# Performance work log

Hardware: AMD Instinct MI355X
Metric: run time of the kernel (lower is better)

## Reference

```python
import jax, jax.numpy as jnp
import numpy as np
from jax import lax

EPS_LN = 1e-5
EPS_NORM = 1e-12

def conv1x1(x, w):
    # x: [b,c,h,w], w: [o,c]
    return jnp.einsum('oc,bchw->bohw', w, x)

def dwconv3x3(x, w):
    # depthwise 3x3, w: [c,1,3,3]
    return lax.conv_general_dilated(
        x, w, window_strides=(1, 1), padding=[(1, 1), (1, 1)],
        feature_group_count=x.shape[1],
        dimension_numbers=('NCHW', 'OIHW', 'NCHW'))

def layernorm_chan(x, w, b):
    # WithBias LayerNorm over channel dim of NCHW (torch does it in b,(hw),c layout)
    mu = jnp.mean(x, axis=1, keepdims=True)
    var = jnp.mean((x - mu) ** 2, axis=1, keepdims=True)
    xn = (x - mu) / jnp.sqrt(var + EPS_LN)
    return xn * w[None, :, None, None] + b[None, :, None, None]

def l2norm(x):
    n = jnp.sqrt(jnp.sum(x * x, axis=-1, keepdims=True))
    return x / jnp.maximum(n, EPS_NORM)

def setup_inputs() -> dict:
    key = jax.random.key(0)
    ks = jax.random.split(key, 8)
    dim, heads, hidden = 64, 2, 170
    b, h, w = 2, 256, 256
    s = 0.05
    return {
        'x': jax.random.normal(ks[0], (b, dim, h, w), jnp.float32),
        'ln1_w': jnp.ones((dim,), jnp.float32),
        'ln1_b': jnp.zeros((dim,), jnp.float32),
        'w_qkv': jax.random.normal(ks[1], (dim * 3, dim), jnp.float32) * s,
        'dw_qkv': jax.random.normal(ks[2], (dim * 3, 1, 3, 3), jnp.float32) * s,
        'temperature': jnp.ones((heads, 1, 1), jnp.float32),
        'w_po': jax.random.normal(ks[3], (dim, dim), jnp.float32) * s,
        'ln2_w': jnp.ones((dim,), jnp.float32),
        'ln2_b': jnp.zeros((dim,), jnp.float32),
        'w_in': jax.random.normal(ks[4], (hidden * 2, dim), jnp.float32) * s,
        'dw_ffn': jax.random.normal(ks[5], (hidden * 2, 1, 3, 3), jnp.float32) * s,
        'w_out': jax.random.normal(ks[6], (dim, hidden), jnp.float32) * s,
    }

def attention(x, w_qkv, dw_qkv, temperature, w_po, num_heads):
    b, c, h, w = x.shape
    qkv = dwconv3x3(conv1x1(x, w_qkv), dw_qkv)            # [b,3c,h,w]
    q, k, v = jnp.split(qkv, 3, axis=1)
    def heads(t):
        return t.reshape(b, num_heads, c // num_heads, h * w)  # [b,hd,ch,hw]
    q, k, v = heads(q), heads(k), heads(v)
    q = l2norm(q)
    k = l2norm(k)
    attn = jnp.einsum('bhcs,bhds->bhcd', q, k) * temperature[None]  # [b,hd,ch,ch]
    attn = jax.nn.softmax(attn, axis=-1)
    out = jnp.einsum('bhcd,bhds->bhcs', attn, v)
    out = out.reshape(b, c, h, w)
    return conv1x1(out, w_po)

def gdfn(x, w_in, dw_ffn, w_out):
    x = dwconv3x3(conv1x1(x, w_in), dw_ffn)
    x1, x2 = jnp.split(x, 2, axis=1)
    return conv1x1(jax.nn.gelu(x1, approximate=False) * x2, w_out)

def reference(x, ln1_w, ln1_b, w_qkv, dw_qkv, temperature, w_po,
              ln2_w, ln2_b, w_in, dw_ffn, w_out):
    num_heads = temperature.shape[0]
    x = x + attention(layernorm_chan(x, ln1_w, ln1_b), w_qkv, dw_qkv,
                      temperature, w_po, num_heads)
    x = x + gdfn(layernorm_chan(x, ln2_w, ln2_b), w_in, dw_ffn, w_out)
    return x
```

## Files before the change

### kernel.cpp

```cpp
#include <hip/hip_runtime.h>
#include <math.h>

#define HW 65536

typedef __attribute__((ext_vector_type(8))) short short8;
typedef __attribute__((ext_vector_type(4))) float floatx4;
typedef __attribute__((ext_vector_type(4))) unsigned short ushortx4;

__device__ __forceinline__ float bf2f(unsigned short u){
  unsigned v = ((unsigned)u)<<16; float f; __builtin_memcpy(&f,&v,4); return f;
}
__device__ __forceinline__ unsigned short f2bf(float f){
  unsigned u; __builtin_memcpy(&u,&f,4);
  u += 0x7fffu + ((u>>16)&1u);
  return (unsigned short)(u>>16);
}
__device__ __forceinline__ int is_f32(const void* magic){
  return ((const unsigned*)magic)[0] == 0x3F800000u;
}
__device__ __forceinline__ float ldv(const void* p, size_t i, int f32){
  return f32 ? ((const float*)p)[i] : bf2f(((const unsigned short*)p)[i]);
}

__global__ __launch_bounds__(64) void k_fold(const void* __restrict__ w_qkv,
                       const void* __restrict__ ln1_w,
                       const void* __restrict__ ln1_b,
                       const void* __restrict__ w_in,
                       const void* __restrict__ ln2_w,
                       const void* __restrict__ ln2_b,
                       const void* __restrict__ w_out,
                       unsigned short* __restrict__ A1, float* __restrict__ a1, float* __restrict__ b1,
                       unsigned short* __restrict__ A5, float* __restrict__ a5, float* __restrict__ b5,
                       unsigned short* __restrict__ A7){
  int f32 = is_f32(ln1_w);
  int bid = blockIdx.x; int c = threadIdx.x;
  if (bid < 192){
    int j = bid;
    float wv = ldv(w_qkv, j*64+c, f32);
    unsigned short q = f2bf(wv*ldv(ln1_w,c,f32));
    A1[j*64+c] = q;
    float sa = bf2f(q);
    float sb = wv*ldv(ln1_b,c,f32);
    #pragma unroll
    for(int o=1;o<64;o<<=1){ sa += __shfl_xor(sa,o,64); sb += __shfl_xor(sb,o,64); }
    if (c==0){ a1[j]=sa; b1[j]=sb; }
  } else if (bid < 576){
    int j = bid-192;
    float wv = (j<340)? ldv(w_in, j*64+c, f32) : 0.f;
    unsigned short q = f2bf(wv*ldv(ln2_w,c,f32));
    A5[j*64+c]=q;
    float sa = bf2f(q);
    float sb = wv*ldv(ln2_b,c,f32);
    #pragma unroll
    for(int o=1;o<64;o<<=1){ sa += __shfl_xor(sa,o,64); sb += __shfl_xor(sb,o,64); }
    if (c==0){ a5[j]=sa; b5[j]=sb; }
  } else {
    int j = bid-576;
    #pragma unroll
    for(int t=0;t<3;t++){
      int k=t*64+c;
      A7[j*192+k] = (k<170)? f2bf(ldv(w_out, j*170+k, f32)) : (unsigned short)0;
    }
  }
}

#define BTT_STR 72
template<int F32>
__device__ __forceinline__ void gemm_ln_body(
    const unsigned short* __restrict__ A, const void* __restrict__ Bv,
    const float* __restrict__ arow, const float* __restrict__ brow,
    unsigned short* __restrict__ out, int outC)
{
  __shared__ unsigned short btt[64*BTT_STR];
  __shared__ float muL[64];
  __shared__ float rsL[64];
  int tid=threadIdx.x; int w=tid>>6, lane=tid&63, m=lane&15, quad=lane>>4;
  int b = blockIdx.x>>8; int s0 = (blockIdx.x<<8)&65535;
  int ch = lane, px0 = w*16;
  short8 afA[3][2]; float ajA[3], bjA[3];
  #pragma unroll
  for(int it=0; it<3; it++){
    int j = (w + it*4)*16 + m;
    const unsigned short* ap = A + j*64 + quad*8;
    afA[it][0] = *(const short8*)ap;
    afA[it][1] = *(const short8*)(ap+32);
    ajA[it] = arow[j]; bjA[it] = brow[j];
  }
  size_t sbase = (size_t)b*64*HW + (size_t)ch*HW + px0;
  floatx4 fr[4]; short8 br0, br1;
  if (F32){
    const float* sp = (const float*)Bv + sbase + s0;
    #pragma unroll
    for(int q4=0;q4<4;q4++) fr[q4] = *(const floatx4*)(sp + q4*4);
  } else {
    const unsigned short* sp = (const unsigned short*)Bv + sbase + s0;
    br0 = *(const short8*)sp; br1 = *(const short8*)(sp+8);
  }
  for(int t=0; t<4; t++){
    int s = s0 + t*64;
    unsigned short tmp[16];
    if (F32){
      #pragma unroll
      for(int q4=0;q4<4;q4++)
        #pragma unroll
        for(int k=0;k<4;k++) tmp[q4*4+k] = f2bf(fr[q4][k]);
    } else {
      #pragma unroll
      for(int jj=0;jj<8;jj++){ tmp[jj]=(unsigned short)br0[jj]; tmp[8+jj]=(unsigned short)br1[jj]; }
    }
    #pragma unroll
    for(int jj=0;jj<16;jj++) btt[(px0+jj)*BTT_STR + ch] = tmp[jj];
    __syncthreads();
    short8 bfr[4][2];
    #pragma unroll
    for(int st4=0; st4<4; st4++){
      const unsigned short* row = btt + (st4*16+m)*BTT_STR + quad*8;
      short8 v0 = *(const short8*)row;
      short8 v1 = *(const short8*)(row+32);
      bfr[st4][0]=v0; bfr[st4][1]=v1;
      float sm=0.f, sq=0.f;
      #pragma unroll
      for(int jj=0;jj<8;jj++){
        float a=bf2f((unsigned short)v0[jj]); sm+=a; sq+=a*a;
        float c=bf2f((unsigned short)v1[jj]); sm+=c; sq+=c*c;
      }
      sm += __shfl_xor(sm,16,64); sq += __shfl_xor(sq,16,64);
      sm += __shfl_xor(sm,32,64); sq += __shfl_xor(sq,32,64);
      float m_ = sm*(1.f/64.f);
      float var = sq*(1.f/64.f) - m_*m_;
      if (w==0 && quad==0){ muL[st4*16+m]=m_; rsL[st4*16+m]=1.f/sqrtf(var+1e-5f); }
    }
    __syncthreads();
    floatx4 mh[4], rh[4];
    #pragma unroll
    for(int st4=0; st4<4; st4++){
      mh[st4] = *(const floatx4*)(muL + st4*16 + quad*4);
      rh[st4] = *(const floatx4*)(rsL + st4*16 + quad*4);
    }
    if (t<3){
      if (F32){
        const float* sp = (const float*)Bv + sbase + s + 64;
        #pragma unroll
        for(int q4=0;q4<4;q4++) fr[q4] = *(const floatx4*)(sp + q4*4);
      } else {
        const unsigned short* sp = (const unsigned short*)Bv + sbase + s + 64;
        br0 = *(const short8*)sp; br1 = *(const short8*)(sp+8);
      }
    }
    #pragma unroll
    for(int it=0; it<3; it++){
      int j = (w + it*4)*16 + m;
      unsigned short* op = out + ((size_t)b*outC + j)*HW + s;
      #pragma unroll
      for(int st4=0; st4<4; st4++){
        floatx4 acc = {0.f,0.f,0.f,0.f};
        acc = __builtin_amdgcn_mfma_f32_16x16x32_bf16(bfr[st4][0], afA[it][0], acc, 0,0,0);
        acc = __builtin_amdgcn_mfma_f32_16x16x32_bf16(bfr[st4][1], afA[it][1], acc, 0,0,0);
        ushortx4 pk;
        #pragma unroll
        for(int r=0;r<4;r++) pk[r] = f2bf(rh[st4][r]*(acc[r] - mh[st4][r]*ajA[it]) + bjA[it]);
        *(ushortx4*)(op + st4*16 + quad*4) = pk;
      }
    }
  }
}
__global__ __launch_bounds__(256) void k_gemm_ln(
    const unsigned short* __restrict__ A, const void* __restrict__ B,
    const float* __restrict__ arow, const float* __restrict__ brow,
    unsigned short* __restrict__ out,
    int outC, const void* __restrict__ magic, int mode)
{
  int f32 = (mode==1) ? 1 : (mode==2 ? 0 : is_f32(magic));
  if (f32) gemm_ln_body<1>(A,B,arow,brow,out,outC);
  else     gemm_ln_body<0>(A,B,arow,brow,out,outC);
}

#define GTT_STR 200
__global__ __launch_bounds__(256) void k_gemm_out(
    const unsigned short* __restrict__ A7, const unsigned short* __restrict__ G,
    const unsigned short* __restrict__ xmid, void* __restrict__ outp, const void* __restrict__ magic)
{
  __shared__ unsigned short gtt[64*GTT_STR];
  int f32 = is_f32(magic);
  int tid=threadIdx.x; int w=tid>>6, lane=tid&63, m=lane&15, quad=lane>>4;
  int b = blockIdx.x>>8; int s0 = (blockIdx.x<<8)&65535;
  int px0 = w*16;
  int j = w*16 + m;
  const unsigned short* ap = A7 + j*192 + quad*8;
  short8 af[6];
  #pragma unroll
  for(int ks=0;ks<6;ks++) af[ks] = *(const short8*)(ap + ks*32);
  const unsigned short* Gb = G + (size_t)b*170*HW + px0;
  size_t ib = ((size_t)b*64 + j)*HW + quad*4;
  short8 sg0[3], sg1[3]; ushortx4 xm[4];
  #pragma unroll
  for(int rep=0; rep<3; rep++){
    const unsigned short* sp = Gb + (size_t)(rep*64 + lane)*HW + s0;
    sg0[rep] = *(const short8*)sp;
    sg1[rep] = *(const short8*)(sp+8);
  }
  #pragma unroll
  for(int st4=0;st4<4;st4++) xm[st4] = *(const ushortx4*)(xmid + ib + s0 + st4*16);
  for(int t=0; t<4; t++){
    int s = s0 + t*64;
    #pragma unroll
    for(int rep=0; rep<3; rep++){
      int ch = rep*64 + lane;
      #pragma unroll
      for(int jj=0;jj<8;jj++){
        gtt[(px0+jj)*GTT_STR + ch]   = (unsigned short)sg0[rep][jj];
        gtt[(px0+8+jj)*GTT_STR + ch] = (unsigned short)sg1[rep][jj];
      }
    }
    __syncthreads();
    short8 sn0[3], sn1[3]; ushortx4 xn[4];
    if (t<3){
      #pragma unroll
      for(int rep=0; rep<3; rep++){
        const unsigned short* sp = Gb + (size_t)(rep*64 + lane)*HW + s + 64;
        sn0[rep] = *(const short8*)sp;
        sn1[rep] = *(const short8*)(sp+8);
      }
      #pragma unroll
      for(int st4=0;st4<4;st4++) xn[st4] = *(const ushortx4*)(xmid + ib + s + 64 + st4*16);
    }
    #pragma unroll
    for(int st4=0; st4<4; st4++){
      const unsigned short* row = gtt + (st4*16+m)*GTT_STR + quad*8;
      floatx4 acc = {0.f,0.f,0.f,0.f};
      #pragma unroll
      for(int ks=0;ks<6;ks++){
        short8 bf = *(const short8*)(row + ks*32);
        acc = __builtin_amdgcn_mfma_f32_16x16x32_bf16(bf, af[ks], acc, 0,0,0);
      }
      size_t idx0 = ib + s + st4*16;
      if (f32){
        floatx4 o;
        #pragma unroll
        for(int r=0;r<4;r++) o[r] = acc[r] + bf2f(xm[st4][r]);
        *(floatx4*)((float*)outp + idx0) = o;
      } else {
        ushortx4 o;
        #pragma unroll
        for(int r=0;r<4;r++) o[r] = f2bf(acc[r] + bf2f(xm[st4][r]));
        *(ushortx4*)((unsigned short*)outp + idx0) = o;
      }
    }
    __syncthreads();
    if (t<3){
      #pragma unroll
      for(int rep=0;rep<3;rep++){ sg0[rep]=sn0[rep]; sg1[rep]=sn1[rep]; }
      #pragma unroll
      for(int st4=0;st4<4;st4++) xm[st4]=xn[st4];
    }
  }
}

__device__ __forceinline__ void conv_row(const float* __restrict__ r0,
    const float* __restrict__ r1, const float* __restrict__ r2,
    const float* __restrict__ w, float* __restrict__ o){
  #pragma unroll
  for(int k=0;k<8;k++){
    o[k] = w[0]*r0[k] + w[1]*r0[k+1] + w[2]*r0[k+2]
         + w[3]*r1[k] + w[4]*r1[k+1] + w[5]*r1[k+2]
         + w[6]*r2[k] + w[7]*r2[k+1] + w[8]*r2[k+2];
  }
}

#define CVT(F, V) { \
    int lv = __shfl((int)(unsigned short)(V)[7], lane-1, 64); \
    int rv = __shfl((int)(unsigned short)(V)[0], lane+1, 64); \
    F[0] = oct       ? bf2f((unsigned short)lv) : 0.f; \
    F[9] = (oct<31)  ? bf2f((unsigned short)rv) : 0.f; \
    _Pragma("unroll") \
    for(int k=0;k<8;k++) F[k+1] = bf2f((unsigned short)(V)[k]); \
  }

__global__ __launch_bounds__(256,4) void k_dwconv(const unsigned short* __restrict__ src,
    const void* __restrict__ wdw, unsigned short* __restrict__ dst, int C,
    const void* __restrict__ magic){
  int f32 = is_f32(magic);
  int tid=threadIdx.x;
  int bc = blockIdx.y;
  int ch = bc % C;
  int lane = tid&63;
  int oct = tid&31, strip = tid>>5;
  int x0 = oct*8;
  int y0 = blockIdx.x*64 + strip*8;
  const unsigned short* sp = src + (size_t)bc*HW;
  short8 R[10];
  #pragma unroll
  for(int r=0;r<10;r++){
    int y = y0-1+r;
    if((unsigned)y<256u) R[r] = *(const short8*)(sp + y*256 + x0);
    else { short8 z = {0,0,0,0,0,0,0,0}; R[r] = z; }
  }
  float w9[9];
  #pragma unroll
  for(int i=0;i<9;i++) w9[i]=ldv(wdw, ch*9+i, f32);
  unsigned short* dp = dst + (size_t)bc*HW + (size_t)y0*256 + x0;
  float A[10],B[10],C_[10],D[10];
  CVT(A, R[0]) CVT(B, R[1]) CVT(C_, R[2])
#define DSTEP(P,Q,Rr) { \
    float o8[8]; \
    conv_row(P,Q,Rr, w9, o8); \
    short8 st; \
    _Pragma("unroll") \
    for(int k=0;k<8;k++) st[k]=(short)f2bf(o8[k]); \
    *(short8*)dp = st; dp += 256; }
  DSTEP(A,B,C_)  CVT(D, R[3])
  DSTEP(B,C_,D)  CVT(A, R[4])
  DSTEP(C_,D,A)  CVT(B, R[5])
  DSTEP(D,A,B)   CVT(C_,R[6])
  DSTEP(A,B,C_)  CVT(D, R[7])
  DSTEP(B,C_,D)  CVT(A, R[8])
  DSTEP(C_,D,A)  CVT(B, R[9])
  DSTEP(D,A,B)
#undef DSTEP
}

__global__ __launch_bounds__(256) void k_ffn_dw(const unsigned short* __restrict__ src,
    const void* __restrict__ wdw, unsigned short* __restrict__ g,
    const void* __restrict__ magic){
  int f32 = is_f32(magic);
  int tid=threadIdx.x;
  int bi = blockIdx.y;
  int b = bi/170, i = bi - b*170;
  int lane = tid&63;
  int oct = tid&31, strip = tid>>5;
  int x0 = oct*8;
  int y0 = blockIdx.x*64 + strip*8;
  const unsigned short* s1 = src + ((size_t)b*340 + i)*HW;
  const unsigned short* s2 = src + ((size_t)b*340 + 170 + i)*HW;
  short8 R1[10], R2[10];
  #pragma unroll
  for(int r=0;r<10;r++){
    int y = y0-1+r;
    if((unsigned)y<256u){
      int o = y*256 + x0;
      R1[r] = *(const short8*)(s1 + o);
      R2[r] = *(const short8*)(s2 + o);
    } else {
      short8 z = {0,0,0,0,0,0,0,0}; R1[r] = z; R2[r] = z;
    }
  }
  float wa[9], wb[9];
  #pragma unroll
  for(int q=0;q<9;q++){ wa[q]=ldv(wdw, i*9+q, f32); wb[q]=ldv(wdw, (i+170)*9+q, f32); }
  unsigned short* gp = g + ((size_t)b*170 + i)*HW + (size_t)y0*256 + x0;
  float A1[10],B1[10],C1[10],D1[10];
  float A2[10],B2[10],C2[10],D2[10];
  CVT(A1, R1[0]) CVT(B1, R1[1]) CVT(C1, R1[2])
  CVT(A2, R2[0]) CVT(B2, R2[1]) CVT(C2, R2[2])
#define CVT2(S, ri) CVT(S##1, R1[ri]) CVT(S##2, R2[ri])
#define FSTEP(P,Q,Rr) { \
    float oa[8], oc[8]; \
    conv_row(P##1,Q##1,Rr##1, wa, oa); \
    conv_row(P##2,Q##2,Rr##2, wb, oc); \
    short8 st; \
    _Pragma("unroll") \
    for(int k=0;k<8;k++){ \
      float u = oa[k]*(1.59576912f + 0.07135481f*oa[k]*oa[k]); \
      float ge = oa[k]/(1.f + __expf(-u)); \
      st[k]=(short)f2bf(ge*oc[k]); \
    } \
    *(short8*)gp = st; gp += 256; }
  FSTEP(A,B,C)  CVT2(D,3)
  FSTEP(B,C,D)  CVT2(A,4)
  FSTEP(C,D,A)  CVT2(B,5)
  FSTEP(D,A,B)  CVT2(C,6)
  FSTEP(A,B,C)  CVT2(D,7)
  FSTEP(B,C,D)  CVT2(A,8)
  FSTEP(C,D,A)  CVT2(B,9)
  FSTEP(D,A,B)
#undef FSTEP
#undef CVT2
}

__global__ __launch_bounds__(256) void k_attn_qk(const unsigned short* __restrict__ qkv,
    float* __restrict__ S, float* __restrict__ qn, float* __restrict__ kn){
  int tid=threadIdx.x; int w=tid>>6, lane=tid&63, m=lane&15, quad=lane>>4;
  int ct=w>>1, dt=w&1;
  int bh=blockIdx.y; int b=bh>>1, hd=bh&1;
  int p0 = blockIdx.x*512;
  const unsigned short* qrow = qkv + ((size_t)(b*192 + hd*32 + ct*16 + m))*HW + p0 + quad*8;
  const unsigned short* krow = qkv + ((size_t)(b*192 + 64 + hd*32 + dt*16 + m))*HW + p0 + quad*8;
  floatx4 acc = {0.f,0.f,0.f,0.f};
  float nq=0.f, nk=0.f;
  for(int it=0; it<16; it++){
    short8 a = *(const short8*)(qrow + it*32);
    short8 bq = *(const short8*)(krow + it*32);
    if (dt==0){
      #pragma unroll
      for(int jj=0;jj<8;jj++){ float v=bf2f((unsigned short)a[jj]); nq+=v*v; }
    }
    if (ct==0){
      #pragma unroll
      for(int jj=0;jj<8;jj++){ float v=bf2f((unsigned short)bq[jj]); nk+=v*v; }
    }
    acc = __builtin_amdgcn_mfma_f32_16x16x32_bf16(a, bq, acc, 0,0,0);
  }
  nq += __shfl_xor(nq,16,64); nq += __shfl_xor(nq,32,64);
  nk += __shfl_xor(nk,16,64); nk += __shfl_xor(nk,32,64);
  if (dt==0 && quad==0) atomicAdd(&qn[bh*32 + ct*16 + m], nq);
  if (ct==0 && quad==0) atomicAdd(&kn[bh*32 + dt*16 + m], nk);
  #pragma unroll
  for(int r=0;r<4;r++)
    atomicAdd(&S[(bh*32 + ct*16 + quad*4 + r)*32 + dt*16 + m], acc[r]);
}

__global__ void k_attn_fin(const float* __restrict__ S, const float* __restrict__ qn,
    const float* __restrict__ kn, const void* __restrict__ temp,
    const void* __restrict__ w_po, unsigned short* __restrict__ Mbf,
    const void* __restrict__ magic){
  int f32 = is_f32(magic);
  __shared__ float attn[2][32][32];
  __shared__ float invq[64], invk[64];
  int b = blockIdx.x; int tid=threadIdx.x;
  if (tid<64){
    int bh=b*2+(tid>>5); int c=tid&31;
    invq[tid] = 1.f/fmaxf(sqrtf(qn[bh*32+c]),1e-12f);
    invk[tid] = 1.f/fmaxf(sqrtf(kn[bh*32+c]),1e-12f);
  }
  __syncthreads();
  if (tid<64){
    int hd=tid>>5, c=tid&31; int bh=b*2+hd;
    float tmp = ldv(temp, hd, f32);
    float row[32]; float mx=-1e30f;
    for(int d=0;d<32;d++){
      float v = S[(bh*32+c)*32+d]*invq[tid]*invk[hd*32+d]*tmp;
      row[d]=v; mx=fmaxf(mx,v);
    }
    float sum=0.f;
    for(int d=0;d<32;d++){ row[d]=expf(row[d]-mx); sum+=row[d]; }
    float inv=1.f/sum;
    for(int d=0;d<32;d++) attn[hd][c][d]=row[d]*inv;
  }
  __syncthreads();
  for(int idx=tid; idx<4096; idx+=256){
    int o=idx>>6, d=idx&63; int hd=d>>5, dd=d&31;
    float sacc=0.f;
    for(int c=0;c<32;c++) sacc += ldv(w_po, o*64 + hd*32 + c, f32) * attn[hd][c][dd];
    Mbf[(size_t)b*4096 + o*64 + d] = f2bf(sacc);
  }
}

#define XSTR 72
__global__ __launch_bounds__(256) void k_attn_ffn(const void* __restrict__ x,
    const unsigned short* __restrict__ qkv, const unsigned short* __restrict__ Mbf,
    unsigned short* __restrict__ xmid,
    const unsigned short* __restrict__ A5, const float* __restrict__ a5, const float* __restrict__ b5,
    unsigned short* __restrict__ ffn_pre, const void* __restrict__ magic){
  __shared__ unsigned short vtt[64*XSTR];
  __shared__ unsigned short xt[64*XSTR];
  __shared__ float muL[64];
  __shared__ float rsL[64];
  int f32 = is_f32(magic);
  int tid=threadIdx.x; int w=tid>>6, lane=tid&63, m=lane&15, quad=lane>>4;
  int b = blockIdx.x>>8; int s0 = (blockIdx.x<<8)&65535;
  int ch = lane, px0 = w*16;
  int jme = w*16 + m;
  const unsigned short* ap = Mbf + (size_t)b*4096 + jme*64 + quad*8;
  short8 af0 = *(const short8*)ap;
  short8 af1 = *(const short8*)(ap+32);
  short8 gA[6][2]; float aj[6], bj[6];
  #pragma unroll
  for(int it=0; it<6; it++){
    int j = (w + it*4)*16 + m;
    const unsigned short* p5 = A5 + j*64 + quad*8;
    gA[it][0] = *(const short8*)p5;
    gA[it][1] = *(const short8*)(p5+32);
    aj[it] = a5[j]; bj[it] = b5[j];
  }
  const unsigned short* vbase = qkv + ((size_t)(b*192 + 128) + ch)*HW + px0;
  size_t xrow = ((size_t)b*64 + jme)*HW + quad*4;
  short8 vr0 = *(const short8*)(vbase + s0);
  short8 vr1 = *(const short8*)(vbase + s0 + 8);
  floatx4 xf[4]; ushortx4 xb[4];
  if (f32){
    const float* xp = (const float*)x + xrow + s0;
    #pragma unroll
    for(int st4=0;st4<4;st4++) xf[st4] = *(const floatx4*)(xp + st4*16);
  } else {
    const unsigned short* xp = (const unsigned short*)x + xrow + s0;
    #pragma unroll
    for(int st4=0;st4<4;st4++) xb[st4] = *(const ushortx4*)(xp + st4*16);
  }
  for(int t=0; t<4; t++){
    int s = s0 + t*64;
    #pragma unroll
    for(int jj=0;jj<8;jj++){
      vtt[(px0+jj)*XSTR + ch]   = (unsigned short)vr0[jj];
      vtt[(px0+8+jj)*XSTR + ch] = (unsigned short)vr1[jj];
    }
    __syncthreads();
    short8 bfr[4][2];
    #pragma unroll
    for(int st4=0; st4<4; st4++){
      const unsigned short* row = vtt + (st4*16+m)*XSTR + quad*8;
      bfr[st4][0] = *(const short8*)row;
      bfr[st4][1] = *(const short8*)(row+32);
    }
    #pragma unroll
    for(int st4=0; st4<4; st4++){
      floatx4 acc = {0.f,0.f,0.f,0.f};
      acc = __builtin_amdgcn_mfma_f32_16x16x32_bf16(bfr[st4][0], af0, acc, 0,0,0);
      acc = __builtin_amdgcn_mfma_f32_16x16x32_bf16(bfr[st4][1], af1, acc, 0,0,0);
      size_t idx0 = xrow + s + st4*16;
      ushortx4 h;
      if (f32){
        #pragma unroll
        for(int r=0;r<4;r++) h[r] = f2bf(acc[r] + xf[st4][r]);
      } else {
        #pragma unroll
        for(int r=0;r<4;r++) h[r] = f2bf(acc[r] + bf2f(xb[st4][r]));
      }
      *(ushortx4*)(xmid + idx0) = h;
      #pragma unroll
      for(int r=0;r<4;r++) xt[(st4*16+quad*4+r)*XSTR + jme] = h[r];
    }
    __syncthreads();
    #pragma unroll
    for(int st4=0; st4<4; st4++){
      const unsigned short* row = xt + (st4*16+m)*XSTR + quad*8;
      short8 v0 = *(const short8*)row;
      short8 v1 = *(const short8*)(row+32);
      bfr[st4][0]=v0; bfr[st4][1]=v1;
      float sm=0.f, sq=0.f;
      #pragma unroll
      for(int jj=0;jj<8;jj++){
        float a=bf2f((unsigned short)v0[jj]); sm+=a; sq+=a*a;
        float c=bf2f((unsigned short)v1[jj]); sm+=c; sq+=c*c;
      }
      sm += __shfl_xor(sm,16,64); sq += __shfl_xor(sq,16,64);
      sm += __shfl_xor(sm,32,64); sq += __shfl_xor(sq,32,64);
      float m_ = sm*(1.f/64.f);
      float var = sq*(1.f/64.f) - m_*m_;
      if (w==0 && quad==0){ muL[st4*16+m]=m_; rsL[st4*16+m]=1.f/sqrtf(var+1e-5f); }
    }
    __syncthreads();
    floatx4 mh[4], rh[4];
    #pragma unroll
    for(int st4=0; st4<4; st4++){
      mh[st4] = *(const floatx4*)(muL + st4*16 + quad*4);
      rh[st4] = *(const floatx4*)(rsL + st4*16 + quad*4);
    }
    if (t<3){
      vr0 = *(const short8*)(vbase + s + 64);
      vr1 = *(const short8*)(vbase + s + 64 + 8);
      if (f32){
        const float* xp = (const float*)x + xrow + s + 64;
        #pragma unroll
        for(int st4=0;st4<4;st4++) xf[st4] = *(const floatx4*)(xp + st4*16);
      } else {
        const unsigned short* xp = (const unsigned short*)x + xrow + s + 64;
        #pragma unroll
        for(int st4=0;st4<4;st4++) xb[st4] = *(const ushortx4*)(xp + st4*16);
      }
    }
    #pragma unroll
    for(int it=0; it<6; it++){
      int j = (w + it*4)*16 + m;
      unsigned short* op = ffn_pre + ((size_t)b*340 + j)*HW + s;
      bool ok = (j < 340);
      #pragma unroll
      for(int st4=0; st4<4; st4++){
        floatx4 acc = {0.f,0.f,0.f,0.f};
        acc = __builtin_amdgcn_mfma_f32_16x16x32_bf16(bfr[st4][0], gA[it][0], acc, 0,0,0);
        acc = __builtin_amdgcn_mfma_f32_16x16x32_bf16(bfr[st4][1], gA[it][1], acc, 0,0,0);
        ushortx4 pk;
        #pragma unroll
        for(int r=0;r<4;r++) pk[r] = f2bf(rh[st4][r]*(acc[r] - mh[st4][r]*aj[it]) + bj[it]);
        if (ok) *(ushortx4*)(op + st4*16 + quad*4) = pk;
      }
    }
  }
}

extern "C" void kernel_launch(void* const* d_in, const int* in_sizes, int n_in,
                              void* d_out, int out_size, void* d_ws, size_t ws_size,
                              hipStream_t stream){
  (void)in_sizes; (void)n_in; (void)out_size; (void)ws_size;
  const void* x     = d_in[0];
  const void* ln1_w = d_in[1];
  const void* ln1_b = d_in[2];
  const void* w_qkv = d_in[3];
  const void* dw_qkv= d_in[4];
  const void* temp  = d_in[5];
  const void* w_po  = d_in[6];
  const void* ln2_w = d_in[7];
  const void* ln2_b = d_in[8];
  const void* w_in  = d_in[9];
  const void* dw_ffn= d_in[10];
  const void* w_out = d_in[11];

  char* ws = (char*)d_ws;
  size_t off = 0;
  auto alloc = [&](size_t n)->void*{ void* p = ws + off; off = (off + n + 255) & ~(size_t)255; return p; };

  unsigned short* A1 = (unsigned short*)alloc(192*64*2);
  float* a1 = (float*)alloc(192*4);
  float* b1 = (float*)alloc(192*4);
  unsigned short* A5 = (unsigned short*)alloc(384*64*2);
  float* a5 = (float*)alloc(384*4);
  float* b5 = (float*)alloc(384*4);
  unsigned short* A7 = (unsigned short*)alloc(64*192*2);
  float* S  = (float*)alloc(4*32*32*4);
  float* qn = (float*)alloc(128*4);
  float* kn = (float*)alloc(128*4);
  unsigned short* Mbf = (unsigned short*)alloc(2*64*64*2);
  unsigned short* xmid = (unsigned short*)alloc((size_t)2*64*HW*2);
  unsigned short* regionA = (unsigned short*)alloc((size_t)2*340*HW*2);
  unsigned short* regionB = (unsigned short*)alloc((size_t)2*192*HW*2);

  k_fold<<<dim3(640), dim3(64), 0, stream>>>(w_qkv, ln1_w, ln1_b, w_in, ln2_w, ln2_b, w_out,
                                             A1, a1, b1, A5, a5, b5, A7);

  k_gemm_ln<<<dim3(512), dim3(256), 0, stream>>>(A1, x, a1, b1, regionA, 192, ln1_w, 0);
  k_dwconv<<<dim3(4,384), dim3(256), 0, stream>>>(regionA, dw_qkv, regionB, 192, ln1_w);

  hipMemsetAsync(S, 0, 16384+512+512, stream);
  k_attn_qk<<<dim3(128,4), dim3(256), 0, stream>>>(regionB, S, qn, kn);
  k_attn_fin<<<dim3(2), dim3(256), 0, stream>>>(S, qn, kn, temp, w_po, Mbf, ln1_w);

  k_attn_ffn<<<dim3(512), dim3(256), 0, stream>>>(x, regionB, Mbf, xmid,
                                                  A5, a5, b5, regionA, ln1_w);
  k_ffn_dw<<<dim3(4,340), dim3(256), 0, stream>>>(regionA, dw_ffn, regionB, ln1_w);
  k_gemm_out<<<dim3(512), dim3(256), 0, stream>>>(A7, regionB, xmid, d_out, ln1_w);
}
```

Before: 277.7 us.

## Fuse LN2 and FFN input projection into the depthwise-conv kernel with a shared-memory row ring

The former attention+FFN kernel is split in two. A lightweight kernel now applies the attention output projection and residual to produce xmid. A new fused kernel then computes LayerNorm2 and the w_in projection per image row on MFMA, keeps three projected rows in a shared-memory ring, and applies the depthwise 3x3 conv and GELU gate directly from that ring. This removes the write and re-read of the large 340-channel intermediate to global memory. In exchange it recomputes halo columns and rows, reads xmid once per channel group, and adds several block barriers per row.

```diff
diff --git a/kernel.cpp b/kernel.cpp
--- a/kernel.cpp
+++ b/kernel.cpp
@@ -319,64 +319,6 @@
 #undef DSTEP
 }
 
-__global__ __launch_bounds__(256) void k_ffn_dw(const unsigned short* __restrict__ src,
-    const void* __restrict__ wdw, unsigned short* __restrict__ g,
-    const void* __restrict__ magic){
-  int f32 = is_f32(magic);
-  int tid=threadIdx.x;
-  int bi = blockIdx.y;
-  int b = bi/170, i = bi - b*170;
-  int lane = tid&63;
-  int oct = tid&31, strip = tid>>5;
-  int x0 = oct*8;
-  int y0 = blockIdx.x*64 + strip*8;
-  const unsigned short* s1 = src + ((size_t)b*340 + i)*HW;
-  const unsigned short* s2 = src + ((size_t)b*340 + 170 + i)*HW;
-  short8 R1[10], R2[10];
-  #pragma unroll
-  for(int r=0;r<10;r++){
-    int y = y0-1+r;
-    if((unsigned)y<256u){
-      int o = y*256 + x0;
-      R1[r] = *(const short8*)(s1 + o);
-      R2[r] = *(const short8*)(s2 + o);
-    } else {
-      short8 z = {0,0,0,0,0,0,0,0}; R1[r] = z; R2[r] = z;
-    }
-  }
-  float wa[9], wb[9];
-  #pragma unroll
-  for(int q=0;q<9;q++){ wa[q]=ldv(wdw, i*9+q, f32); wb[q]=ldv(wdw, (i+170)*9+q, f32); }
-  unsigned short* gp = g + ((size_t)b*170 + i)*HW + (size_t)y0*256 + x0;
-  float A1[10],B1[10],C1[10],D1[10];
-  float A2[10],B2[10],C2[10],D2[10];
-  CVT(A1, R1[0]) CVT(B1, R1[1]) CVT(C1, R1[2])
-  CVT(A2, R2[0]) CVT(B2, R2[1]) CVT(C2, R2[2])
-#define CVT2(S, ri) CVT(S##1, R1[ri]) CVT(S##2, R2[ri])
-#define FSTEP(P,Q,Rr) { \
-    float oa[8], oc[8]; \
-    conv_row(P##1,Q##1,Rr##1, wa, oa); \
-    conv_row(P##2,Q##2,Rr##2, wb, oc); \
-    short8 st; \
-    _Pragma("unroll") \
-    for(int k=0;k<8;k++){ \
-      float u = oa[k]*(1.59576912f + 0.07135481f*oa[k]*oa[k]); \
-      float ge = oa[k]/(1.f + __expf(-u)); \
-      st[k]=(short)f2bf(ge*oc[k]); \
-    } \
-    *(short8*)gp = st; gp += 256; }
-  FSTEP(A,B,C)  CVT2(D,3)
-  FSTEP(B,C,D)  CVT2(A,4)
-  FSTEP(C,D,A)  CVT2(B,5)
-  FSTEP(D,A,B)  CVT2(C,6)
-  FSTEP(A,B,C)  CVT2(D,7)
-  FSTEP(B,C,D)  CVT2(A,8)
-  FSTEP(C,D,A)  CVT2(B,9)
-  FSTEP(D,A,B)
-#undef FSTEP
-#undef CVT2
-}
-
 __global__ __launch_bounds__(256) void k_attn_qk(const unsigned short* __restrict__ qkv,
     float* __restrict__ S, float* __restrict__ qn, float* __restrict__ kn){
   int tid=threadIdx.x; int w=tid>>6, lane=tid&63, m=lane&15, quad=lane>>4;
@@ -446,133 +388,194 @@
 }
 
 #define XSTR 72
-__global__ __launch_bounds__(256) void k_attn_ffn(const void* __restrict__ x,
+__global__ __launch_bounds__(256) void k_attn_mv(const void* __restrict__ x,
     const unsigned short* __restrict__ qkv, const unsigned short* __restrict__ Mbf,
-    unsigned short* __restrict__ xmid,
-    const unsigned short* __restrict__ A5, const float* __restrict__ a5, const float* __restrict__ b5,
-    unsigned short* __restrict__ ffn_pre, const void* __restrict__ magic){
+    unsigned short* __restrict__ xmid, const void* __restrict__ magic){
   __shared__ unsigned short vtt[64*XSTR];
-  __shared__ unsigned short xt[64*XSTR];
-  __shared__ float muL[64];
-  __shared__ float rsL[64];
   int f32 = is_f32(magic);
   int tid=threadIdx.x; int w=tid>>6, lane=tid&63, m=lane&15, quad=lane>>4;
-  int b = blockIdx.x>>8; int s0 = (blockIdx.x<<8)&65535;
+  int sblk = blockIdx.x*64; int b=sblk>>16, s=sblk&65535;
   int ch = lane, px0 = w*16;
+  const unsigned short* vp = qkv + ((size_t)(b*192 + 128) + ch)*HW + s + px0;
+  short8 vr0 = *(const short8*)vp;
+  short8 vr1 = *(const short8*)(vp+8);
   int jme = w*16 + m;
   const unsigned short* ap = Mbf + (size_t)b*4096 + jme*64 + quad*8;
   short8 af0 = *(const short8*)ap;
   short8 af1 = *(const short8*)(ap+32);
-  short8 gA[6][2]; float aj[6], bj[6];
-  #pragma unroll
-  for(int it=0; it<6; it++){
-    int j = (w + it*4)*16 + m;
-    const unsigned short* p5 = A5 + j*64 + quad*8;
-    gA[it][0] = *(const short8*)p5;
-    gA[it][1] = *(const short8*)(p5+32);
-    aj[it] = a5[j]; bj[it] = b5[j];
-  }
-  const unsigned short* vbase = qkv + ((size_t)(b*192 + 128) + ch)*HW + px0;
-  size_t xrow = ((size_t)b*64 + jme)*HW + quad*4;
-  short8 vr0 = *(const short8*)(vbase + s0);
-  short8 vr1 = *(const short8*)(vbase + s0 + 8);
-  floatx4 xf[4]; ushortx4 xb[4];
+  size_t xi0 = ((size_t)b*64 + jme)*HW + s + quad*4;
+  floatx4 xf[4]; ushortx4 xb2[4];
   if (f32){
-    const float* xp = (const float*)x + xrow + s0;
-    #pragma unroll
-    for(int st4=0;st4<4;st4++) xf[st4] = *(const floatx4*)(xp + st4*16);
+    #pragma unroll
+    for(int st4=0;st4<4;st4++) xf[st4] = *(const floatx4*)((const float*)x + xi0 + st4*16);
   } else {
-    const unsigned short* xp = (const unsigned short*)x + xrow + s0;
-    #pragma unroll
-    for(int st4=0;st4<4;st4++) xb[st4] = *(const ushortx4*)(xp + st4*16);
-  }
-  for(int t=0; t<4; t++){
-    int s = s0 + t*64;
-    #pragma unroll
-    for(int jj=0;jj<8;jj++){
-      vtt[(px0+jj)*XSTR + ch]   = (unsigned short)vr0[jj];
-      vtt[(px0+8+jj)*XSTR + ch] = (unsigned short)vr1[jj];
-    }
-    __syncthreads();
-    short8 bfr[4][2];
-    #pragma unroll
-    for(int st4=0; st4<4; st4++){
-      const unsigned short* row = vtt + (st4*16+m)*XSTR + quad*8;
-      bfr[st4][0] = *(const short8*)row;
-      bfr[st4][1] = *(const short8*)(row+32);
-    }
-    #pragma unroll
-    for(int st4=0; st4<4; st4++){
-      floatx4 acc = {0.f,0.f,0.f,0.f};
-      acc = __builtin_amdgcn_mfma_f32_16x16x32_bf16(bfr[st4][0], af0, acc, 0,0,0);
-      acc = __builtin_amdgcn_mfma_f32_16x16x32_bf16(bfr[st4][1], af1, acc, 0,0,0);
-      size_t idx0 = xrow + s + st4*16;
-      ushortx4 h;
-      if (f32){
-        #pragma unroll
-        for(int r=0;r<4;r++) h[r] = f2bf(acc[r] + xf[st4][r]);
-      } else {
-        #pragma unroll
-        for(int r=0;r<4;r++) h[r] = f2bf(acc[r] + bf2f(xb[st4][r]));
-      }
-      *(ushortx4*)(xmid + idx0) = h;
-      #pragma unroll
-      for(int r=0;r<4;r++) xt[(st4*16+quad*4+r)*XSTR + jme] = h[r];
-    }
-    __syncthreads();
-    #pragma unroll
-    for(int st4=0; st4<4; st4++){
-      const unsigned short* row = xt + (st4*16+m)*XSTR + quad*8;
+    #pragma unroll
+    for(int st4=0;st4<4;st4++) xb2[st4] = *(const ushortx4*)((const unsigned short*)x + xi0 + st4*16);
+  }
+  #pragma unroll
+  for(int jj=0;jj<8;jj++){
+    vtt[(px0+jj)*XSTR + ch]   = (unsigned short)vr0[jj];
+    vtt[(px0+8+jj)*XSTR + ch] = (unsigned short)vr1[jj];
+  }
+  __syncthreads();
+  #pragma unroll
+  for(int st4=0; st4<4; st4++){
+    const unsigned short* row = vtt + (st4*16+m)*XSTR + quad*8;
+    short8 b0 = *(const short8*)row;
+    short8 b1 = *(const short8*)(row+32);
+    floatx4 acc = {0.f,0.f,0.f,0.f};
+    acc = __builtin_amdgcn_mfma_f32_16x16x32_bf16(b0, af0, acc, 0,0,0);
+    acc = __builtin_amdgcn_mfma_f32_16x16x32_bf16(b1, af1, acc, 0,0,0);
+    ushortx4 h;
+    if (f32){
+      #pragma unroll
+      for(int r=0;r<4;r++) h[r] = f2bf(acc[r] + xf[st4][r]);
+    } else {
+      #pragma unroll
+      for(int r=0;r<4;r++) h[r] = f2bf(acc[r] + bf2f(xb2[st4][r]));
+    }
+    *(ushortx4*)(xmid + xi0 + st4*16) = h;
+  }
+}
+
+#define FF_XS 72
+#define FF_RS 88
+#define FF_CH 68
+#define FF_R  16
+__global__ __launch_bounds__(320) void k_ffn_fused(
+    const unsigned short* __restrict__ xmid,
+    const void* __restrict__ wdw,
+    const unsigned short* __restrict__ A5, const float* __restrict__ a5, const float* __restrict__ b5,
+    unsigned short* __restrict__ gated, const void* __restrict__ magic)
+{
+  __shared__ unsigned short xstage[80*FF_XS];
+  __shared__ unsigned short ring[3][FF_CH][FF_RS];
+  __shared__ float muL[80], rsL[80];
+  int f32 = is_f32(magic);
+  int tid = threadIdx.x;
+  int w = tid>>6, lane = tid&63, m = lane&15, quad = lane>>4;
+  int bi = blockIdx.x;
+  int g = bi % 5; bi /= 5;
+  int xt = bi & 3; bi >>= 2;
+  int yt = bi & 15; int b = bi >> 4;
+  int x0 = xt*64;
+  int y0 = yt*FF_R;
+  int jg = w*16 + m;
+  int r5 = (jg<34) ? g*34+jg : (jg<68 ? 136 + g*34 + jg : 340 + (jg-68));
+  const unsigned short* ap = A5 + r5*64 + quad*8;
+  short8 af0 = *(const short8*)ap;
+  short8 af1 = *(const short8*)(ap+32);
+  float aj = a5[r5], bj = b5[r5];
+  int c = tid>>3, o = tid&7;
+  float wa[9], wb[9];
+  if (tid < 272){
+    int i = g*34 + c;
+    #pragma unroll
+    for(int q=0;q<9;q++){ wa[q]=ldv(wdw, i*9+q, f32); wb[q]=ldv(wdw, (i+170)*9+q, f32); }
+  }
+  const unsigned short* xb = xmid + (size_t)b*64*HW;
+  unsigned short* gb = gated + ((size_t)b*170 + (size_t)(g*34))*HW;
+  for(int s=0; s<FF_R+2; s++){
+    int yr = y0 - 1 + s;
+    int valid = ((unsigned)yr < 256u);
+    int slot = s % 3;
+    short8 lr0, lr1;
+    if (valid){
+      const unsigned short* sp = xb + (size_t)lane*HW + yr*256 + (x0-8) + w*16;
+      lr0 = *(const short8*)sp;
+      lr1 = *(const short8*)(sp+8);
+    }
+    __syncthreads();
+    if (valid){
+      #pragma unroll
+      for(int jj=0;jj<8;jj++){
+        xstage[(w*16+jj)*FF_XS + lane]   = (unsigned short)lr0[jj];
+        xstage[(w*16+8+jj)*FF_XS + lane] = (unsigned short)lr1[jj];
+      }
+    }
+    __syncthreads();
+    if (valid){
+      const unsigned short* row = xstage + (w*16+m)*FF_XS + quad*8;
       short8 v0 = *(const short8*)row;
       short8 v1 = *(const short8*)(row+32);
-      bfr[st4][0]=v0; bfr[st4][1]=v1;
       float sm=0.f, sq=0.f;
       #pragma unroll
       for(int jj=0;jj<8;jj++){
         float a=bf2f((unsigned short)v0[jj]); sm+=a; sq+=a*a;
-        float c=bf2f((unsigned short)v1[jj]); sm+=c; sq+=c*c;
+        float c2=bf2f((unsigned short)v1[jj]); sm+=c2; sq+=c2*c2;
       }
       sm += __shfl_xor(sm,16,64); sq += __shfl_xor(sq,16,64);
       sm += __shfl_xor(sm,32,64); sq += __shfl_xor(sq,32,64);
       float m_ = sm*(1.f/64.f);
       float var = sq*(1.f/64.f) - m_*m_;
-      if (w==0 && quad==0){ muL[st4*16+m]=m_; rsL[st4*16+m]=1.f/sqrtf(var+1e-5f); }
-    }
-    __syncthreads();
-    floatx4 mh[4], rh[4];
-    #pragma unroll
-    for(int st4=0; st4<4; st4++){
-      mh[st4] = *(const floatx4*)(muL + st4*16 + quad*4);
-      rh[st4] = *(const floatx4*)(rsL + st4*16 + quad*4);
-    }
-    if (t<3){
-      vr0 = *(const short8*)(vbase + s + 64);
-      vr1 = *(const short8*)(vbase + s + 64 + 8);
-      if (f32){
-        const float* xp = (const float*)x + xrow + s + 64;
-        #pragma unroll
-        for(int st4=0;st4<4;st4++) xf[st4] = *(const floatx4*)(xp + st4*16);
-      } else {
-        const unsigned short* xp = (const unsigned short*)x + xrow + s + 64;
-        #pragma unroll
-        for(int st4=0;st4<4;st4++) xb[st4] = *(const ushortx4*)(xp + st4*16);
-      }
-    }
-    #pragma unroll
-    for(int it=0; it<6; it++){
-      int j = (w + it*4)*16 + m;
-      unsigned short* op = ffn_pre + ((size_t)b*340 + j)*HW + s;
-      bool ok = (j < 340);
-      #pragma unroll
-      for(int st4=0; st4<4; st4++){
+      if (quad==0){ muL[w*16+m]=m_; rsL[w*16+m]=1.f/sqrtf(var+1e-5f); }
+    }
+    __syncthreads();
+    if (valid){
+      #pragma unroll
+      for(int pt=0; pt<5; pt++){
+        const unsigned short* row = xstage + (pt*16+m)*FF_XS + quad*8;
+        short8 b0 = *(const short8*)row;
+        short8 b1 = *(const short8*)(row+32);
         floatx4 acc = {0.f,0.f,0.f,0.f};
-        acc = __builtin_amdgcn_mfma_f32_16x16x32_bf16(bfr[st4][0], gA[it][0], acc, 0,0,0);
-        acc = __builtin_amdgcn_mfma_f32_16x16x32_bf16(bfr[st4][1], gA[it][1], acc, 0,0,0);
-        ushortx4 pk;
-        #pragma unroll
-        for(int r=0;r<4;r++) pk[r] = f2bf(rh[st4][r]*(acc[r] - mh[st4][r]*aj[it]) + bj[it]);
-        if (ok) *(ushortx4*)(op + st4*16 + quad*4) = pk;
-      }
+        acc = __builtin_amdgcn_mfma_f32_16x16x32_bf16(b0, af0, acc, 0,0,0);
+        acc = __builtin_amdgcn_mfma_f32_16x16x32_bf16(b1, af1, acc, 0,0,0);
+        floatx4 m4 = *(const floatx4*)(muL + pt*16 + quad*4);
+        floatx4 r4 = *(const floatx4*)(rsL + pt*16 + quad*4);
+        if (jg < FF_CH){
+          ushortx4 pk;
+          #pragma unroll
+          for(int r=0;r<4;r++){
+            int p = pt*16 + quad*4 + r;
+            int xx = x0 - 8 + p;
+            float vv = r4[r]*(acc[r] - m4[r]*aj) + bj;
+            pk[r] = ((unsigned)xx < 256u) ? f2bf(vv) : (unsigned short)0;
+          }
+          *(ushortx4*)(&ring[slot][jg][pt*16 + quad*4]) = pk;
+        }
+      }
+    } else {
+      unsigned* zp = (unsigned*)(&ring[slot][0][0]);
+      for(int idx=tid; idx<(FF_CH*FF_RS/2); idx+=320) zp[idx] = 0u;
+    }
+    __syncthreads();
+    if (s>=2 && tid<272){
+      int yo = y0 + s - 2;
+      int sl0=(s-2)%3, sl1=(s-1)%3, sl2=slot;
+      float oa[8], oc[8];
+      #pragma unroll
+      for(int k=0;k<8;k++){ oa[k]=0.f; oc[k]=0.f; }
+#define ROWACC(SL, WR) { \
+      const unsigned short* b1p = &ring[SL][c][8*o]; \
+      const unsigned short* b2p = &ring[SL][34+c][8*o]; \
+      short8 ra = *(const short8*)b1p; short8 rb = *(const short8*)(b1p+8); \
+      float f[10]; \
+      f[0]=bf2f((unsigned short)ra[7]); \
+      _Pragma("unroll") \
+      for(int jj=0;jj<8;jj++) f[1+jj]=bf2f((unsigned short)rb[jj]); \
+      f[9]=bf2f(b1p[16]); \
+      _Pragma("unroll") \
+      for(int k=0;k<8;k++) oa[k] += wa[WR*3+0]*f[k] + wa[WR*3+1]*f[k+1] + wa[WR*3+2]*f[k+2]; \
+      short8 rc = *(const short8*)b2p; short8 rd = *(const short8*)(b2p+8); \
+      f[0]=bf2f((unsigned short)rc[7]); \
+      _Pragma("unroll") \
+      for(int jj=0;jj<8;jj++) f[1+jj]=bf2f((unsigned short)rd[jj]); \
+      f[9]=bf2f(b2p[16]); \
+      _Pragma("unroll") \
+      for(int k=0;k<8;k++) oc[k] += wb[WR*3+0]*f[k] + wb[WR*3+1]*f[k+1] + wb[WR*3+2]*f[k+2]; \
+    }
+      ROWACC(sl0, 0)
+      ROWACC(sl1, 1)
+      ROWACC(sl2, 2)
+#undef ROWACC
+      short8 st;
+      #pragma unroll
+      for(int k=0;k<8;k++){
+        float u = oa[k]*(1.59576912f + 0.07135481f*oa[k]*oa[k]);
+        float ge = oa[k]/(1.f + __expf(-u));
+        st[k]=(short)f2bf(ge*oc[k]);
+      }
+      *(short8*)(gb + (size_t)c*HW + yo*256 + x0 + o*8) = st;
     }
   }
 }
@@ -623,8 +626,7 @@
   k_attn_qk<<<dim3(128,4), dim3(256), 0, stream>>>(regionB, S, qn, kn);
   k_attn_fin<<<dim3(2), dim3(256), 0, stream>>>(S, qn, kn, temp, w_po, Mbf, ln1_w);
 
-  k_attn_ffn<<<dim3(512), dim3(256), 0, stream>>>(x, regionB, Mbf, xmid,
-                                                  A5, a5, b5, regionA, ln1_w);
-  k_ffn_dw<<<dim3(4,340), dim3(256), 0, stream>>>(regionA, dw_ffn, regionB, ln1_w);
+  k_attn_mv<<<dim3(2048), dim3(256), 0, stream>>>(x, regionB, Mbf, xmid, ln1_w);
+  k_ffn_fused<<<dim3(640), dim3(320), 0, stream>>>(xmid, dw_ffn, A5, a5, b5, regionB, ln1_w);
   k_gemm_out<<<dim3(512), dim3(256), 0, stream>>>(A7, regionB, xmid, d_out, ln1_w);
 }
```

Measured after the change: 375.1 us. +35.1%, slower.
